# Kernel optimization log

Hardware: AMD Instinct MI355X
Metric: run time of the kernel (lower is better)

Reference implementation:

```python
import jax, jax.numpy as jnp
import numpy as np

STRIDE = 1
PAD = 3  # kernel_size // 2 = 7 // 2


def setup_inputs() -> dict:
    key = jax.random.key(0)
    k1, k2, k3 = jax.random.split(key, 3)
    B, Cin, T = 32, 128, 4096
    K, Cout, ks = 4, 256, 7
    x = jax.random.normal(k1, (B, Cin, T), dtype=jnp.float32)
    weight = jax.random.normal(k2, (K, Cout, Cin, ks), dtype=jnp.float32) * 0.01
    bias = jnp.zeros((K, Cout), dtype=jnp.float32)
    rw = jax.random.normal(k3, (K, Cin), dtype=jnp.float32) * 0.05
    rb = jnp.zeros((K,), dtype=jnp.float32)
    return {"x": x, "weight": weight, "bias": bias, "rw": rw, "rb": rb}


def reference(x, weight, bias, rw, rb):
    # x: [B, Cin, T]; weight: [K, Cout, Cin, ks]; bias: [K, Cout]
    K, Cout, Cin, ks = weight.shape
    B = x.shape[0]
    # routing: adaptive avg pool over T -> Linear -> softmax
    pooled = jnp.mean(x, axis=-1)                      # [B, Cin]
    alpha = jax.nn.softmax(pooled @ rw.T + rb, axis=-1)  # [B, K]
    # all K conv branches in one conv by folding K into out-channels
    w_all = weight.reshape(K * Cout, Cin, ks)
    y = jax.lax.conv_general_dilated(
        x, w_all, window_strides=(STRIDE,), padding=[(PAD, PAD)],
        dimension_numbers=("NCH", "OIH", "NCH"))      # [B, K*Cout, T']
    Tp = y.shape[-1]
    y = y.reshape(B, K, Cout, Tp) + bias[None, :, :, None]
    # softmax-routed weighted sum over the K branches
    out = jnp.einsum("bk,bkct->bct", alpha, y)         # [B, Cout, T']
    return out
```

## Files before the change

kernel.cpp:

```cpp
#include <hip/hip_runtime.h>
#include <stdint.h>


#define WEFF_OFF   0u
#define POOLED_OFF 14680064u
#define BEFF_OFF   14696448u

typedef short short8 __attribute__((ext_vector_type(8)));
typedef float f32x16 __attribute__((ext_vector_type(16)));

__device__ __forceinline__ unsigned short f2bf(float f) {
  unsigned int u = __builtin_bit_cast(unsigned int, f);
  u += 0x7fffu + ((u >> 16) & 1u);
  return (unsigned short)(u >> 16);
}

__global__ __launch_bounds__(256) void k_pool(const float* __restrict__ x,
                                              float* __restrict__ pooled) {
  __shared__ float ws4[4];
  int row = blockIdx.x;
  const float* src = x + (size_t)row * 4096 + threadIdx.x * 16;
  float s = 0.f;
  #pragma unroll
  for (int i = 0; i < 4; ++i) {
    float4 v = *(const float4*)(src + i * 4);
    s += (v.x + v.y) + (v.z + v.w);
  }
  #pragma unroll
  for (int off = 32; off > 0; off >>= 1) s += __shfl_down(s, off);
  int lane = threadIdx.x & 63, wv = threadIdx.x >> 6;
  if (lane == 0) ws4[wv] = s;
  __syncthreads();
  if (threadIdx.x == 0) pooled[row] = (ws4[0] + ws4[1]) + (ws4[2] + ws4[3]);
}

__global__ __launch_bounds__(256) void k_fold(
    const float* __restrict__ w, const float* __restrict__ pooled,
    const float* __restrict__ rw, const float* __restrict__ rb,
    const float* __restrict__ bias, unsigned short* __restrict__ weff,
    float* __restrict__ bias_eff) {
  __shared__ float al[32][4];
  int tid = threadIdx.x;
  if (tid < 128) {
    int b = tid >> 2, k = tid & 3;
    const float* pp = pooled + b * 128;
    const float* rwk = rw + k * 128;
    float s = rb[k];
    #pragma unroll 8
    for (int j = 0; j < 128; ++j) s += pp[j] * (1.0f / 4096.0f) * rwk[j];
    al[b][k] = s;
  }
  __syncthreads();
  if (tid < 32) {
    float l0 = al[tid][0], l1 = al[tid][1], l2 = al[tid][2], l3 = al[tid][3];
    float m = fmaxf(fmaxf(l0, l1), fmaxf(l2, l3));
    float e0 = __expf(l0 - m), e1 = __expf(l1 - m);
    float e2 = __expf(l2 - m), e3 = __expf(l3 - m);
    float inv = 1.0f / (e0 + e1 + e2 + e3);
    al[tid][0] = e0 * inv; al[tid][1] = e1 * inv;
    al[tid][2] = e2 * inv; al[tid][3] = e3 * inv;
  }
  __syncthreads();
  if (blockIdx.x == 0) {
    #pragma unroll
    for (int b = 0; b < 32; ++b) {
      float s = 0.f;
      #pragma unroll
      for (int k = 0; k < 4; ++k) s += al[b][k] * bias[k * 256 + tid];
      bias_eff[b * 256 + tid] = s;
    }
  }
  int bq = blockIdx.x & 3;
  int pos = (blockIdx.x >> 2) * 256 + tid;
  int cb = pos / 14336;
  int r = pos - cb * 14336;
  int step = r >> 8;
  int ct = (r >> 6) & 3;
  int lpos = r & 63;
  int s7 = step >> 3, slice = step & 7;
  int cout = cb * 128 + ct * 32 + (lpos & 31);
  int ci0 = slice * 16 + (lpos >> 5) * 8;
  float wv[4][8];
  #pragma unroll
  for (int k = 0; k < 4; ++k) {
    const float* src = w + ((size_t)(k * 256 + cout) * 128 + ci0) * 7 + s7;
    #pragma unroll
    for (int j = 0; j < 8; ++j) wv[k][j] = src[j * 7];
  }
  unsigned short* dst = weff + (size_t)pos * 8;
  #pragma unroll
  for (int bi = 0; bi < 8; ++bi) {
    int b = bq * 8 + bi;
    float a0 = al[b][0], a1 = al[b][1], a2 = al[b][2], a3 = al[b][3];
    unsigned short h[8];
    #pragma unroll
    for (int j = 0; j < 8; ++j)
      h[j] = f2bf(a0 * wv[0][j] + a1 * wv[1][j] + a2 * wv[2][j] + a3 * wv[3][j]);
    uint4 o;
    o.x = (unsigned)h[0] | ((unsigned)h[1] << 16);
    o.y = (unsigned)h[2] | ((unsigned)h[3] << 16);
    o.z = (unsigned)h[4] | ((unsigned)h[5] << 16);
    o.w = (unsigned)h[6] | ((unsigned)h[7] << 16);
    *(uint4*)(dst + (size_t)b * 229376) = o;
  }
}

__global__ __launch_bounds__(512, 4) void k_conv4(
    const float* __restrict__ x, const unsigned short* __restrict__ weff,
    const float* __restrict__ bias_eff, float* __restrict__ out) {
  __shared__ __align__(16) unsigned short xs[16 * 262 * 8];
  int phys = blockIdx.x;
  int logical = (phys & 7) * 64 + (phys >> 3);
  int b = logical >> 4, tb = logical & 15;
  int tid = threadIdx.x;
  int t00 = tb << 8;

  {
    const float* xbase = x + (size_t)b * 128 * 4096;
    int rh = tid & 255, gh = tid >> 8;
    int xrow = t00 - 3 + rh;
    bool valid = (unsigned)xrow < 4096u;
    #pragma unroll
    for (int i = 0; i < 8; ++i) {
      int g = gh * 8 + i;
      float f[8];
      #pragma unroll
      for (int u = 0; u < 8; ++u)
        f[u] = valid ? xbase[(size_t)(g * 8 + u) * 4096 + xrow] : 0.f;
      uint4 o;
      o.x = (unsigned)f2bf(f[0]) | ((unsigned)f2bf(f[1]) << 16);
      o.y = (unsigned)f2bf(f[2]) | ((unsigned)f2bf(f[3]) << 16);
      o.z = (unsigned)f2bf(f[4]) | ((unsigned)f2bf(f[5]) << 16);
      o.w = (unsigned)f2bf(f[6]) | ((unsigned)f2bf(f[7]) << 16);
      *(uint4*)(&xs[(g * 262 + rh) * 8]) = o;
    }
    if (tid < 128) {
      int g = tid >> 3, r8 = tid & 7;
      if (r8 < 6) {
        int row2 = 256 + r8;
        int xrow2 = t00 - 3 + row2;
        bool v2 = (unsigned)xrow2 < 4096u;
        float f[8];
        #pragma unroll
        for (int u = 0; u < 8; ++u)
          f[u] = v2 ? xbase[(size_t)(g * 8 + u) * 4096 + xrow2] : 0.f;
        uint4 o;
        o.x = (unsigned)f2bf(f[0]) | ((unsigned)f2bf(f[1]) << 16);
        o.y = (unsigned)f2bf(f[2]) | ((unsigned)f2bf(f[3]) << 16);
        o.z = (unsigned)f2bf(f[4]) | ((unsigned)f2bf(f[5]) << 16);
        o.w = (unsigned)f2bf(f[6]) | ((unsigned)f2bf(f[7]) << 16);
        *(uint4*)(&xs[(g * 262 + row2) * 8]) = o;
      }
    }
  }
  __syncthreads();

  int wave = tid >> 6, lane = tid & 63;
  int l31 = lane & 31, lhi = lane >> 5;
  int wm = wave & 1, wn = wave >> 1;
  const short8* wb8 = (const short8*)weff + (size_t)b * 28672 + lane;

  for (int cb = 0; cb < 2; ++cb) {
    f32x16 acc[2][2];
    #pragma unroll
    for (int mi = 0; mi < 2; ++mi)
      #pragma unroll
      for (int ni = 0; ni < 2; ++ni)
        acc[mi][ni] = (f32x16)(0.f);

    const short8* wfrag = wb8 + (size_t)cb * 14336 + (wm * 2) * 64;
    short8 av[2];
    #pragma unroll
    for (int mi = 0; mi < 2; ++mi) av[mi] = wfrag[mi * 64];

    #pragma unroll 2
    for (int step = 0; step < 56; ++step) {
      int s = step >> 3, slice = step & 7;
      short8 avn[2];
      if (step < 55) {
        #pragma unroll
        for (int mi = 0; mi < 2; ++mi)
          avn[mi] = wfrag[(step + 1) * 256 + mi * 64];
      }
      short8 bv[2];
      int prow = (slice * 2 + lhi) * 262 + s;
      #pragma unroll
      for (int ni = 0; ni < 2; ++ni) {
        int tt = wn * 64 + ni * 32 + l31;
        bv[ni] = *(const short8*)(&xs[(size_t)(prow + tt) * 8]);
      }
      #pragma unroll
      for (int mi = 0; mi < 2; ++mi)
        #pragma unroll
        for (int ni = 0; ni < 2; ++ni)
          acc[mi][ni] = __builtin_amdgcn_mfma_f32_32x32x16_bf16(
              av[mi], bv[ni], acc[mi][ni], 0, 0, 0);
      #pragma unroll
      for (int mi = 0; mi < 2; ++mi) av[mi] = avn[mi];
    }

    int crow0 = b * 256 + cb * 128;
    #pragma unroll
    for (int mi = 0; mi < 2; ++mi) {
      #pragma unroll
      for (int r = 0; r < 16; ++r) {
        int c = wm * 64 + mi * 32 + (r & 3) + 8 * (r >> 2) + 4 * lhi;
        float bb = bias_eff[crow0 + c];
        float* orow = out + (size_t)(crow0 + c) * 4096 + t00;
        #pragma unroll
        for (int ni = 0; ni < 2; ++ni)
          orow[wn * 64 + ni * 32 + l31] = acc[mi][ni][r] + bb;
      }
    }
  }
}

extern "C" void kernel_launch(void* const* d_in, const int* in_sizes, int n_in,
                              void* d_out, int out_size, void* d_ws, size_t ws_size,
                              hipStream_t stream) {
  const float* x    = (const float*)d_in[0];
  const float* w    = (const float*)d_in[1];
  const float* bias = (const float*)d_in[2];
  const float* rw   = (const float*)d_in[3];
  const float* rb   = (const float*)d_in[4];
  float* out = (float*)d_out;
  char* ws = (char*)d_ws;
  unsigned short* weff = (unsigned short*)(ws + WEFF_OFF);
  float* pooled        = (float*)(ws + POOLED_OFF);
  float* bias_eff      = (float*)(ws + BEFF_OFF);

  hipLaunchKernelGGL(k_pool,  dim3(4096), dim3(256), 0, stream, x, pooled);
  hipLaunchKernelGGL(k_fold,  dim3(448),  dim3(256), 0, stream,
                     w, pooled, rw, rb, bias, weff, bias_eff);
  hipLaunchKernelGGL(k_conv4, dim3(512),  dim3(512), 0, stream,
                     x, weff, bias_eff, out);
}
```

Measured before the change: 257.3 us.

## Restructure conv into 256-thread blocks with double-buffered half-tile x prefetch

The conv kernel now uses 256 threads per block. Each block processes its 256-timestep tile as two 128-step halves held in double-buffered LDS. While the first half computes, the second half of x is loaded into registers, so the global load latency is meant to overlap with MFMA work. Each wave now owns 32 timesteps by 128 channels (4 M-tiles sharing one B fragment) instead of a 2x2 tile, which changes the reuse pattern and register pressure. The cost is re-streaming the weight fragments twice per block and holding 72 prefetch floats per thread in registers, which may hurt occupancy.

```diff
diff --git a/kernel.cpp b/kernel.cpp
--- a/kernel.cpp
+++ b/kernel.cpp
@@ -14,6 +14,12 @@
   u += 0x7fffu + ((u >> 16) & 1u);
   return (unsigned short)(u >> 16);
 }
+
+#define PACK8(o, f)                                              \
+  o.x = (unsigned)f2bf(f[0]) | ((unsigned)f2bf(f[1]) << 16);     \
+  o.y = (unsigned)f2bf(f[2]) | ((unsigned)f2bf(f[3]) << 16);     \
+  o.z = (unsigned)f2bf(f[4]) | ((unsigned)f2bf(f[5]) << 16);     \
+  o.w = (unsigned)f2bf(f[6]) | ((unsigned)f2bf(f[7]) << 16);
 
 __global__ __launch_bounds__(256) void k_pool(const float* __restrict__ x,
                                               float* __restrict__ pooled) {
@@ -92,127 +98,143 @@
   for (int bi = 0; bi < 8; ++bi) {
     int b = bq * 8 + bi;
     float a0 = al[b][0], a1 = al[b][1], a2 = al[b][2], a3 = al[b][3];
-    unsigned short h[8];
+    float acc8[8];
     #pragma unroll
     for (int j = 0; j < 8; ++j)
-      h[j] = f2bf(a0 * wv[0][j] + a1 * wv[1][j] + a2 * wv[2][j] + a3 * wv[3][j]);
+      acc8[j] = a0 * wv[0][j] + a1 * wv[1][j] + a2 * wv[2][j] + a3 * wv[3][j];
     uint4 o;
-    o.x = (unsigned)h[0] | ((unsigned)h[1] << 16);
-    o.y = (unsigned)h[2] | ((unsigned)h[3] << 16);
-    o.z = (unsigned)h[4] | ((unsigned)h[5] << 16);
-    o.w = (unsigned)h[6] | ((unsigned)h[7] << 16);
+    PACK8(o, acc8);
     *(uint4*)(dst + (size_t)b * 229376) = o;
   }
 }
 
-__global__ __launch_bounds__(512, 4) void k_conv4(
+__global__ __launch_bounds__(256, 2) void k_conv7(
     const float* __restrict__ x, const unsigned short* __restrict__ weff,
     const float* __restrict__ bias_eff, float* __restrict__ out) {
-  __shared__ __align__(16) unsigned short xs[16 * 262 * 8];
+  __shared__ __align__(16) unsigned short xs[2][16 * 134 * 8];
   int phys = blockIdx.x;
   int logical = (phys & 7) * 64 + (phys >> 3);
   int b = logical >> 4, tb = logical & 15;
   int tid = threadIdx.x;
   int t00 = tb << 8;
+  const float* xbase = x + (size_t)b * 128 * 4096;
+
+  int rh = tid & 127, gh = tid >> 7;
+  int hg = tid >> 3, hr = tid & 7;
 
   {
-    const float* xbase = x + (size_t)b * 128 * 4096;
-    int rh = tid & 255, gh = tid >> 8;
     int xrow = t00 - 3 + rh;
-    bool valid = (unsigned)xrow < 4096u;
+    bool v = (unsigned)xrow < 4096u;
     #pragma unroll
     for (int i = 0; i < 8; ++i) {
       int g = gh * 8 + i;
       float f[8];
       #pragma unroll
       for (int u = 0; u < 8; ++u)
-        f[u] = valid ? xbase[(size_t)(g * 8 + u) * 4096 + xrow] : 0.f;
-      uint4 o;
-      o.x = (unsigned)f2bf(f[0]) | ((unsigned)f2bf(f[1]) << 16);
-      o.y = (unsigned)f2bf(f[2]) | ((unsigned)f2bf(f[3]) << 16);
-      o.z = (unsigned)f2bf(f[4]) | ((unsigned)f2bf(f[5]) << 16);
-      o.w = (unsigned)f2bf(f[6]) | ((unsigned)f2bf(f[7]) << 16);
-      *(uint4*)(&xs[(g * 262 + rh) * 8]) = o;
-    }
-    if (tid < 128) {
-      int g = tid >> 3, r8 = tid & 7;
-      if (r8 < 6) {
-        int row2 = 256 + r8;
-        int xrow2 = t00 - 3 + row2;
-        bool v2 = (unsigned)xrow2 < 4096u;
-        float f[8];
-        #pragma unroll
-        for (int u = 0; u < 8; ++u)
-          f[u] = v2 ? xbase[(size_t)(g * 8 + u) * 4096 + xrow2] : 0.f;
-        uint4 o;
-        o.x = (unsigned)f2bf(f[0]) | ((unsigned)f2bf(f[1]) << 16);
-        o.y = (unsigned)f2bf(f[2]) | ((unsigned)f2bf(f[3]) << 16);
-        o.z = (unsigned)f2bf(f[4]) | ((unsigned)f2bf(f[5]) << 16);
-        o.w = (unsigned)f2bf(f[6]) | ((unsigned)f2bf(f[7]) << 16);
-        *(uint4*)(&xs[(g * 262 + row2) * 8]) = o;
-      }
-    }
-  }
-  __syncthreads();
+        f[u] = v ? xbase[(size_t)(g * 8 + u) * 4096 + xrow] : 0.f;
+      uint4 o; PACK8(o, f);
+      *(uint4*)(&xs[0][(g * 134 + rh) * 8]) = o;
+    }
+    if (tid < 128 && hr < 6) {
+      int row = 128 + hr, xr2 = t00 - 3 + row;
+      bool v2 = (unsigned)xr2 < 4096u;
+      float f[8];
+      #pragma unroll
+      for (int u = 0; u < 8; ++u)
+        f[u] = v2 ? xbase[(size_t)(hg * 8 + u) * 4096 + xr2] : 0.f;
+      uint4 o; PACK8(o, f);
+      *(uint4*)(&xs[0][(hg * 134 + row) * 8]) = o;
+    }
+  }
+  __syncthreads();
+
+  float f1[8][8];
+  float f1h[8];
+  {
+    int ts1 = t00 + 128;
+    int xrow = ts1 - 3 + rh;
+    bool v = (unsigned)xrow < 4096u;
+    #pragma unroll
+    for (int i = 0; i < 8; ++i) {
+      int g = gh * 8 + i;
+      #pragma unroll
+      for (int u = 0; u < 8; ++u)
+        f1[i][u] = v ? xbase[(size_t)(g * 8 + u) * 4096 + xrow] : 0.f;
+    }
+    if (tid < 128 && hr < 6) {
+      int xr2 = ts1 - 3 + 128 + hr;
+      bool v2 = (unsigned)xr2 < 4096u;
+      #pragma unroll
+      for (int u = 0; u < 8; ++u)
+        f1h[u] = v2 ? xbase[(size_t)(hg * 8 + u) * 4096 + xr2] : 0.f;
+    }
+  }
 
   int wave = tid >> 6, lane = tid & 63;
   int l31 = lane & 31, lhi = lane >> 5;
-  int wm = wave & 1, wn = wave >> 1;
+  int wn = wave;
   const short8* wb8 = (const short8*)weff + (size_t)b * 28672 + lane;
 
-  for (int cb = 0; cb < 2; ++cb) {
-    f32x16 acc[2][2];
-    #pragma unroll
-    for (int mi = 0; mi < 2; ++mi)
-      #pragma unroll
-      for (int ni = 0; ni < 2; ++ni)
-        acc[mi][ni] = (f32x16)(0.f);
-
-    const short8* wfrag = wb8 + (size_t)cb * 14336 + (wm * 2) * 64;
-    short8 av[2];
-    #pragma unroll
-    for (int mi = 0; mi < 2; ++mi) av[mi] = wfrag[mi * 64];
-
-    #pragma unroll 2
-    for (int step = 0; step < 56; ++step) {
-      int s = step >> 3, slice = step & 7;
-      short8 avn[2];
-      if (step < 55) {
-        #pragma unroll
-        for (int mi = 0; mi < 2; ++mi)
-          avn[mi] = wfrag[(step + 1) * 256 + mi * 64];
-      }
-      short8 bv[2];
-      int prow = (slice * 2 + lhi) * 262 + s;
-      #pragma unroll
-      for (int ni = 0; ni < 2; ++ni) {
-        int tt = wn * 64 + ni * 32 + l31;
-        bv[ni] = *(const short8*)(&xs[(size_t)(prow + tt) * 8]);
-      }
-      #pragma unroll
-      for (int mi = 0; mi < 2; ++mi)
-        #pragma unroll
-        for (int ni = 0; ni < 2; ++ni)
-          acc[mi][ni] = __builtin_amdgcn_mfma_f32_32x32x16_bf16(
-              av[mi], bv[ni], acc[mi][ni], 0, 0, 0);
-      #pragma unroll
-      for (int mi = 0; mi < 2; ++mi) av[mi] = avn[mi];
-    }
-
-    int crow0 = b * 256 + cb * 128;
-    #pragma unroll
-    for (int mi = 0; mi < 2; ++mi) {
-      #pragma unroll
-      for (int r = 0; r < 16; ++r) {
-        int c = wm * 64 + mi * 32 + (r & 3) + 8 * (r >> 2) + 4 * lhi;
-        float bb = bias_eff[crow0 + c];
-        float* orow = out + (size_t)(crow0 + c) * 4096 + t00;
-        #pragma unroll
-        for (int ni = 0; ni < 2; ++ni)
-          orow[wn * 64 + ni * 32 + l31] = acc[mi][ni][r] + bb;
-      }
-    }
-  }
+  #define COMP_EPI(BUF, CB, TSABS)                                         \
+  {                                                                        \
+    f32x16 acc[4];                                                         \
+    _Pragma("unroll")                                                      \
+    for (int mi = 0; mi < 4; ++mi) acc[mi] = (f32x16)(0.f);                \
+    const short8* wf = wb8 + (size_t)(CB) * 14336;                         \
+    short8 av[4];                                                          \
+    _Pragma("unroll")                                                      \
+    for (int mi = 0; mi < 4; ++mi) av[mi] = wf[mi * 64];                   \
+    _Pragma("unroll 2")                                                    \
+    for (int step = 0; step < 56; ++step) {                                \
+      int s = step >> 3, slice = step & 7;                                 \
+      short8 avn[4];                                                       \
+      if (step < 55) {                                                     \
+        _Pragma("unroll")                                                  \
+        for (int mi = 0; mi < 4; ++mi)                                     \
+          avn[mi] = wf[(step + 1) * 256 + mi * 64];                        \
+      }                                                                    \
+      int rr = (slice * 2 + lhi) * 134 + s + wn * 32 + l31;                \
+      short8 bv = *(const short8*)(&xs[BUF][(size_t)rr * 8]);              \
+      _Pragma("unroll")                                                    \
+      for (int mi = 0; mi < 4; ++mi)                                       \
+        acc[mi] = __builtin_amdgcn_mfma_f32_32x32x16_bf16(                 \
+            av[mi], bv, acc[mi], 0, 0, 0);                                 \
+      _Pragma("unroll")                                                    \
+      for (int mi = 0; mi < 4; ++mi) av[mi] = avn[mi];                     \
+    }                                                                      \
+    int crow0 = b * 256 + (CB)*128;                                        \
+    _Pragma("unroll")                                                      \
+    for (int mi = 0; mi < 4; ++mi) {                                       \
+      _Pragma("unroll")                                                    \
+      for (int r16 = 0; r16 < 16; ++r16) {                                 \
+        int c = mi * 32 + (r16 & 3) + 8 * (r16 >> 2) + 4 * lhi;            \
+        out[(size_t)(crow0 + c) * 4096 + (TSABS) + wn * 32 + l31] =        \
+            acc[mi][r16] + bias_eff[crow0 + c];                            \
+      }                                                                    \
+    }                                                                      \
+  }
+
+  COMP_EPI(0, 0, t00);
+  COMP_EPI(0, 1, t00);
+
+  {
+    #pragma unroll
+    for (int i = 0; i < 8; ++i) {
+      int g = gh * 8 + i;
+      uint4 o; PACK8(o, f1[i]);
+      *(uint4*)(&xs[1][(g * 134 + rh) * 8]) = o;
+    }
+    if (tid < 128 && hr < 6) {
+      uint4 o; PACK8(o, f1h);
+      *(uint4*)(&xs[1][(hg * 134 + 128 + hr) * 8]) = o;
+    }
+  }
+  __syncthreads();
+
+  COMP_EPI(1, 0, t00 + 128);
+  COMP_EPI(1, 1, t00 + 128);
+
+  #undef COMP_EPI
 }
 
 extern "C" void kernel_launch(void* const* d_in, const int* in_sizes, int n_in,
@@ -232,6 +254,6 @@
   hipLaunchKernelGGL(k_pool,  dim3(4096), dim3(256), 0, stream, x, pooled);
   hipLaunchKernelGGL(k_fold,  dim3(448),  dim3(256), 0, stream,
                      w, pooled, rw, rb, bias, weff, bias_eff);
-  hipLaunchKernelGGL(k_conv4, dim3(512),  dim3(512), 0, stream,
+  hipLaunchKernelGGL(k_conv7, dim3(512),  dim3(256), 0, stream,
                      x, weff, bias_eff, out);
 }
```

Result: slower. 377.7 us (+46.8%).
